# Optimization experiments

Measured on AMD Instinct MI355X. Metric: run time of the kernel, lower is better.

The kernel has to match this reference:

```python
import jax, jax.numpy as jnp
import numpy as np
import math

B, L, D, H, FACTOR = 4, 2048, 256, 8, 5
DH = D // H

def setup_inputs() -> dict:
    key = jax.random.key(0)
    ks = jax.random.split(key, 12)
    s = 1.0 / math.sqrt(D)
    return {
        "q": jax.random.normal(ks[0], (B, L, D), jnp.float32),
        "k": jax.random.normal(ks[1], (B, L, D), jnp.float32),
        "v": jax.random.normal(ks[2], (B, L, D), jnp.float32),
        "Wq": jax.random.normal(ks[3], (D, D), jnp.float32) * s,
        "bq": jax.random.normal(ks[4], (D,), jnp.float32) * s,
        "Wk": jax.random.normal(ks[5], (D, D), jnp.float32) * s,
        "bk": jax.random.normal(ks[6], (D,), jnp.float32) * s,
        "Wv": jax.random.normal(ks[7], (D, D), jnp.float32) * s,
        "bv": jax.random.normal(ks[8], (D,), jnp.float32) * s,
        "Wc": jax.random.normal(ks[9], (D, D), jnp.float32) * s,
        "bc": jax.random.normal(ks[10], (D,), jnp.float32) * s,
        "index_sample": jax.random.randint(ks[11], (L,), 0, L),  # U_part = min(5*L*ceil(log1p(L)), L) = L
    }

def reference(q, k, v, Wq, bq, Wk, bk, Wv, bv, Wc, bc, index_sample):
    # projections (torch Linear: x @ W^T + b)
    qp = q @ Wq.T + bq
    kp = k @ Wk.T + bk
    vp = v @ Wv.T + bv
    # NOTE: original reshapes q with a raw view (no transpose), k/v via split()
    q4 = qp.reshape(B, H, L, DH)                       # faithful to q.view(B, H, L, dh)
    k4 = kp.reshape(B, L, H, DH).transpose(0, 2, 1, 3)
    v4 = vp.reshape(B, L, H, DH).transpose(0, 2, 1, 3)
    qf = q4.reshape(B * H, L, DH)
    kf = k4.reshape(B * H, L, DH)
    vf = v4.reshape(B * H, L, DH)
    # random K sampling (with replacement); U_part == L here
    K_sample = kf[:, index_sample, :]                  # [BH, L, dh]
    QK = jnp.einsum('bld,bud->blu', qf, K_sample)      # [BH, L, L]
    M = QK.max(axis=-1) - QK.sum(axis=-1) / L          # sparsity measure [BH, L]
    u = min(FACTOR * math.ceil(math.log1p(L)), L)      # = 40
    _, top_idx = jax.lax.top_k(-M, u)                  # topk(..., largest=False)
    Q_red = jnp.take_along_axis(qf, top_idx[:, :, None], axis=1)  # [BH, u, dh]
    scores = jnp.einsum('bud,bld->bul', Q_red, kf) / math.sqrt(DH)
    probs = jax.nn.softmax(scores, axis=-1)
    out = jnp.einsum('bul,bld->bud', probs, vf)        # [BH, u, dh]
    out = out.reshape(B, H, u, DH).transpose(0, 2, 1, 3).reshape(B, u, D)
    return out @ Wc.T + bc
```

## Files before the change

kernel.cpp:

```cpp
#include <hip/hip_runtime.h>
#include <math.h>

#define B_ 4
#define L_ 2048
#define D_ 256
#define H_ 8
#define DH_ 32
#define NH_ 32
#define U_ 40
#define LD_ 524288

typedef __attribute__((ext_vector_type(8))) short short8;
typedef __attribute__((ext_vector_type(4))) float floatx4;

static __device__ __forceinline__ unsigned long long ullmin_(unsigned long long a, unsigned long long b) {
    return a < b ? a : b;
}
static __device__ __forceinline__ unsigned short f2bf_rne(float x) {
    unsigned u = __float_as_uint(x);
    unsigned r = u + 0x7FFFu + ((u >> 16) & 1u);
    return (unsigned short)(r >> 16);
}
static __device__ __forceinline__ float bf2f(unsigned short h) {
    return __uint_as_float(((unsigned)h) << 16);
}
// ... 106 lines not shown

#pragma unroll
    for (int mt = 0; mt < 2; ++mt)
#pragma unroll
        for (int nt = 0; nt < 4; ++nt) {
            const int c = colBase + nt * 16 + lq;
            const float bv_ = bias[c];
#pragma unroll
            for (int r = 0; r < 4; ++r) {
                const int mr = rowBaseW + mt * 16 + quad * 4 + r;
                Y[(size_t)mr * 256 + c] = acc[mt][nt][r] + bv_;
            }
        }
}

__global__ __launch_bounds__(256) void gemm_out(const float* __restrict__ X,
                                                const float* __restrict__ Wc,
                                                const float* __restrict__ bias,
                                                float* __restrict__ Y) {
    const int t = threadIdx.x;
    const int w = t >> 6, lane = t & 63;
    const int lq = lane & 15, quad = lane >> 4;
    const int colBase = blockIdx.y * 64;
    const int rowBaseW = blockIdx.x * 128 + w * 32;

    __shared__ unsigned short Bls[24576];

    floatx4 acc[2][4];
#pragma unroll
    for (int mt = 0; mt < 2; ++mt)
#pragma unroll
        for (int nt = 0; nt < 4; ++nt) acc[mt][nt] = (floatx4){0.f, 0.f, 0.f, 0.f};

    for (int phase = 0; phase < 2; ++phase) {
        __syncthreads();
#pragma unroll
        for (int r = 0; r < 8; ++r) {
            const int e = t + 256 * r;
            const int col = e >> 5;
            const int k4u = e & 31;
            const int kk = phase * 128 + k4u * 4;
            const float4 x = *(const float4*)(Wc + (size_t)(colBase + col) * 256 + kk);
            float xs[4] = {x.x, x.y, x.z, x.w};
            unsigned short hv[4], mv4[4], lv[4];
#pragma unroll
            for (int j = 0; j < 4; ++j) {
                hv[j] = f2bf_rne(xs[j]);
// ... 2 lines not shown
                const float e2 = e1 - bf2f(mv4[j]);
                lv[j] = f2bf_rne(e2);
            }
            const int nt = col >> 4, cin = col & 15;
            const int ktl = k4u >> 3, kin = (k4u & 7) * 4;
            const int base = nt * 512 + cin * 32 + kin;
            *(ushort4*)&Bls[((0 * 4 + ktl) << 11) + base] = make_ushort4(hv[0], hv[1], hv[2], hv[3]);
            *(ushort4*)&Bls[((1 * 4 + ktl) << 11) + base] = make_ushort4(mv4[0], mv4[1], mv4[2], mv4[3]);
            *(ushort4*)&Bls[((2 * 4 + ktl) << 11) + base] = make_ushort4(lv[0], lv[1], lv[2], lv[3]);
        }
        __syncthreads();

#pragma unroll
        for (int ktl = 0; ktl < 4; ++ktl) {
            const int kt = phase * 4 + ktl;
            short8 Bh[4], Bm[4], Bl[4];
            const int fo = lq * 32 + quad * 8;
#pragma unroll
            for (int j = 0; j < 4; ++j) {
                Bh[j] = *(const short8*)&Bls[((0 * 4 + ktl) << 11) + j * 512 + fo];
                Bm[j] = *(const short8*)&Bls[((1 * 4 + ktl) << 11) + j * 512 + fo];
                Bl[j] = *(const short8*)&Bls[((2 * 4 + ktl) << 11) + j * 512 + fo];
            }
#pragma unroll
            for (int mt = 0; mt < 2; ++mt) {
                const int m = rowBaseW + mt * 16 + lq;
                short8 Ah, Am, Al;
                {
                    float xs[8] = {0.f, 0.f, 0.f, 0.f, 0.f, 0.f, 0.f, 0.f};
                    if (m < 160) {
                        const float* xr = X + (size_t)m * 256 + kt * 32 + quad * 8;
                        const float4 x0 = *(const float4*)xr;
                        const float4 x1 = *(const float4*)(xr + 4);
                        xs[0] = x0.x; xs[1] = x0.y; xs[2] = x0.z; xs[3] = x0.w;
                        xs[4] = x1.x; xs[5] = x1.y; xs[6] = x1.z; xs[7] = x1.w;
                    }
#pragma unroll
                    for (int j = 0; j < 8; ++j) {
                        const unsigned short h = f2bf_rne(xs[j]);
                        const float e1 = xs[j] - bf2f(h);
                        const unsigned short md = f2bf_rne(e1);
                        const float e2 = e1 - bf2f(md);
                        Ah[j] = (short)h;
                        Am[j] = (short)md;
                        Al[j] = (short)f2bf_rne(e2);
                    }
                }
#pragma unroll
                for (int j = 0; j < 4; ++j) {
                    floatx4 a = acc[mt][j];
                    a = __builtin_amdgcn_mfma_f32_16x16x32_bf16(Am, Bm[j], a, 0, 0, 0);
                    a = __builtin_amdgcn_mfma_f32_16x16x32_bf16(Ah, Bl[j], a, 0, 0, 0);
                    a = __builtin_amdgcn_mfma_f32_16x16x32_bf16(Al, Bh[j], a, 0, 0, 0);
                    a = __builtin_amdgcn_mfma_f32_16x16x32_bf16(Ah, Bm[j], a, 0, 0, 0);
                    a = __builtin_amdgcn_mfma_f32_16x16x32_bf16(Am, Bh[j], a, 0, 0, 0);
                    a = __builtin_amdgcn_mfma_f32_16x16x32_bf16(Ah, Bh[j], a, 0, 0, 0);
                    acc[mt][j] = a;
                }
            }
        }
    }

#pragma unroll
    for (int mt = 0; mt < 2; ++mt)
#pragma unroll
        for (int nt = 0; nt < 4; ++nt) {
            const int c = colBase + nt * 16 + lq;
            const float bv = bias[c];
#pragma unroll
            for (int r = 0; r < 4; ++r) {
                const int mr = rowBaseW + mt * 16 + quad * 4 + r;
                if (mr < 160) Y[(size_t)mr * 256 + c] = acc[mt][nt][r] + bv;
            }
        }
}

__global__ __launch_bounds__(256) void kconv_ksum(const float* __restrict__ kp,
                                                  const int* __restrict__ idx,
                                                  unsigned short* __restrict__ Khi,
                                                  unsigned short* __restrict__ Klo,
                                                  float* __restrict__ Ksum8) {
    const int blk = blockIdx.x;
    const int i = blk >> 3, uc = blk & 7;
    const int b = i >> 3, h = i & 7;
    const int t = threadIdx.x;
    const int dq = (t & 7) * 4;
    const int ur = t >> 3;

    __shared__ float part[32][36];
    float ksum[4] = {0.f, 0.f, 0.f, 0.f};

#pragma unroll
    for (int p = 0; p < 8; ++p) {
        int u = uc * 256 + p * 32 + ur;
        const float4 x = *(const float4*)(kp + (size_t)b * LD_ + (size_t)idx[u] * D_ + h * DH_ + dq);
        float xs[4] = {x.x, x.y, x.z, x.w};
        unsigned short hv[4], lv[4];
#pragma unroll
        for (int j = 0; j < 4; ++j) {
            ksum[j] += xs[j];
            hv[j] = f2bf_rne(xs[j]);
            lv[j] = f2bf_rne(xs[j] - bf2f(hv[j]));
        }
        size_t o = ((size_t)i * 2048 + u) * 32 + dq;
        *(ushort4*)(Khi + o) = make_ushort4(hv[0], hv[1], hv[2], hv[3]);
        *(ushort4*)(Klo + o) = make_ushort4(lv[0], lv[1], lv[2], lv[3]);
    }
#pragma unroll
    for (int j = 0; j < 4; ++j) part[ur][dq + j] = ksum[j];
    __syncthreads();
    if (t < 32) {
        float s = 0.f;
#pragma unroll 8
        for (int u2 = 0; u2 < 32; ++u2) s += part[u2][t];
        Ksum8[(size_t)blk * 32 + t] = s;
    }
}

__global__ __launch_bounds__(256) void mpart_mfma(const float* __restrict__ qp,
                                                  const unsigned short* __restrict__ Khi,
                                                  const unsigned short* __restrict__ Klo,
                                                  const float* __restrict__ Ksum8,
                                                  float* __restrict__ Mv,
                                                  float* __restrict__ Qmean) {
    const int blk = blockIdx.x;
    const int i = blk >> 5;
    const int lg = blk & 31;
    const int t = threadIdx.x;
    const int w = t >> 6;
    const int lane = t & 63;
    const int lq = lane & 15;
    const int quad = lane >> 4;

    __shared__ float ssum[32];
    __shared__ float red[4][64];
    if (t < 32) {
        float s = 0.f;
#pragma unroll
        for (int uc = 0; uc < 8; ++uc) s += Ksum8[((size_t)i * 8 + uc) * 32 + t];
        ssum[t] = s;
    }

    short8 Ah[4], Al[4];
#pragma unroll
    for (int lt = 0; lt < 4; ++lt) {
        const int l = lg * 64 + lt * 16 + lq;
        const float* qrow = qp + ((size_t)i * 2048 + l) * 32 + quad * 8;
        float4 x0 = *(const float4*)(qrow);
        float4 x1 = *(const float4*)(qrow + 4);
        float xs[8] = {x0.x, x0.y, x0.z, x0.w, x1.x, x1.y, x1.z, x1.w};
#pragma unroll
        for (int j = 0; j < 8; ++j) {
            unsigned short h = f2bf_rne(xs[j]);
            unsigned short lo = f2bf_rne(xs[j] - bf2f(h));
            Ah[lt][j] = (short)h;
            Al[lt][j] = (short)lo;
        }
    }

    floatx4 rmax[4];
#pragma unroll
    for (int lt = 0; lt < 4; ++lt)
        rmax[lt] = (floatx4){-INFINITY, -INFINITY, -INFINITY, -INFINITY};

    const size_t kfrag = ((size_t)i * 2048 + w * 512 + lq) * 32 + quad * 8;
    const unsigned short* ph = Khi + kfrag;
    const unsigned short* pl = Klo + kfrag;
#pragma unroll 2
    for (int s = 0; s < 32; ++s) {
        short8 Bh = *(const short8*)(ph + (size_t)s * 512);
        short8 Bl = *(const short8*)(pl + (size_t)s * 512);
#pragma unroll
        for (int lt = 0; lt < 4; ++lt) {
            floatx4 acc = (floatx4){0.f, 0.f, 0.f, 0.f};
            acc = __builtin_amdgcn_mfma_f32_16x16x32_bf16(Al[lt], Bh, acc, 0, 0, 0);
            acc = __builtin_amdgcn_mfma_f32_16x16x32_bf16(Ah[lt], Bl, acc, 0, 0, 0);
            acc = __builtin_amdgcn_mfma_f32_16x16x32_bf16(Ah[lt], Bh, acc, 0, 0, 0);
#pragma unroll
            for (int r = 0; r < 4; ++r) rmax[lt][r] = fmaxf(rmax[lt][r], acc[r]);
        }
    }

#pragma unroll
    for (int lt = 0; lt < 4; ++lt)
#pragma unroll
        for (int r = 0; r < 4; ++r) {
            float v = rmax[lt][r];
#pragma unroll
            for (int off = 1; off < 16; off <<= 1)
                v = fmaxf(v, __shfl_xor(v, off, 64));
            rmax[lt][r] = v;
        }
    if (lq == 0) {
#pragma unroll
        for (int lt = 0; lt < 4; ++lt)
#pragma unroll
            for (int r = 0; r < 4; ++r)
                red[w][lt * 16 + quad * 4 + r] = rmax[lt][r];
    }
    __syncthreads();
    if (t < 64) {
        const int l = lg * 64 + t;
        float m = fmaxf(fmaxf(red[0][t], red[1][t]), fmaxf(red[2][t], red[3][t]));
        const float4* q4 = (const float4*)(qp + ((size_t)i * 2048 + l) * 32);
        const float4* s4 = (const float4*)ssum;
        float qs = 0.f;
#pragma unroll
        for (int z = 0; z < 8; ++z) {
            float4 a = q4[z];
            float4 c = s4[z];
            qs = fmaf(a.x, c.x, qs);
            qs = fmaf(a.y, c.y, qs);
            qs = fmaf(a.z, c.z, qs);
            qs = fmaf(a.w, c.w, qs);
        }
        const float qm = qs * (1.0f / 2048.0f);
        Qmean[(size_t)i * 2048 + l] = qm;
        Mv[(size_t)i * 2048 + l] = m - qm;
    }
}

__global__ __launch_bounds__(256) void topk64_kernel(const float* __restrict__ Mv,
                                                     int* __restrict__ candIdx) {
    const int i = blockIdx.x;
    const int t = threadIdx.x;
    unsigned long long keys[8];
    __shared__ unsigned long long wred[4];
#pragma unroll
    for (int j = 0; j < 8; ++j) {
        const int l = t + 256 * j;
        unsigned u32 = __float_as_uint(Mv[(size_t)i * 2048 + l]);
        u32 = (u32 & 0x80000000u) ? ~u32 : (u32 | 0x80000000u);
        keys[j] = ((unsigned long long)u32 << 32) | (unsigned)l;
    }
    for (int it = 0; it < 64; ++it) {
        unsigned long long best = keys[0];
#pragma unroll
        for (int j = 1; j < 8; ++j) best = ullmin_(best, keys[j]);
#pragma unroll
        for (int off = 1; off < 64; off <<= 1)
            best = ullmin_(best, __shfl_xor(best, off, 64));
        if ((t & 63) == 0) wred[t >> 6] = best;
        __syncthreads();
        const unsigned long long m = ullmin_(ullmin_(wred[0], wred[1]), ullmin_(wred[2], wred[3]));
        if (t == 0) candIdx[i * 64 + it] = (int)(m & 0xffffffffu);
#pragma unroll
        for (int j = 0; j < 8; ++j)
            if (keys[j] == m) keys[j] = ~0ULL;
        __syncthreads();
    }
}

__global__ __launch_bounds__(256) void refine_kernel(const float* __restrict__ qp,
                                                     const float* __restrict__ kp,
                                                     const int* __restrict__ idx,
                                                     const int* __restrict__ candIdx,
                                                     float* __restrict__ refPart) {
    const int blk = blockIdx.x;
    const int i = blk >> 3, c = blk & 7;
    const int b = i >> 3, h = i & 7;
    const int t = threadIdx.x;
    __shared__ float qc[64][40];
    __shared__ float Ks[128][40];

    {
        const int cand = t >> 2, dp = (t & 3) * 8;
        const int l = candIdx[i * 64 + cand];
        const float* src = qp + ((size_t)i * 2048 + l) * 32 + dp;
        *(float4*)&qc[cand][dp] = *(const float4*)(src);
        *(float4*)&qc[cand][dp + 4] = *(const float4*)(src + 4);
    }
    __syncthreads();

    const int cand = t >> 2, usub = t & 3;
    float qv[32];
#pragma unroll
    for (int z = 0; z < 8; ++z) {
        float4 a = *(const float4*)&qc[cand][z * 4];
        qv[4 * z] = a.x; qv[4 * z + 1] = a.y; qv[4 * z + 2] = a.z; qv[4 * z + 3] = a.w;
    }

    float m = -INFINITY;
    for (int s = 0; s < 2; ++s) {
        {
            const int r = t >> 1, half = t & 1;
            const int u = c * 256 + s * 128 + r;
            const float* krow = kp + (size_t)b * LD_ + (size_t)idx[u] * D_ + h * DH_ + half * 16;
#pragma unroll
            for (int z = 0; z < 4; ++z)
                *(float4*)&Ks[r][half * 16 + z * 4] = *(const float4*)(krow + z * 4);
        }
        __syncthreads();
        for (int ur = usub; ur < 128; ur += 4) {
            float a0 = 0, a1 = 0, a2 = 0, a3 = 0;
#pragma unroll
            for (int z = 0; z < 8; ++z) {
                float4 kv = *(const float4*)&Ks[ur][z * 4];
                a0 = fmaf(qv[4 * z], kv.x, a0);
                a1 = fmaf(qv[4 * z + 1], kv.y, a1);
                a2 = fmaf(qv[4 * z + 2], kv.z, a2);
                a3 = fmaf(qv[4 * z + 3], kv.w, a3);
            }
            m = fmaxf(m, (a0 + a1) + (a2 + a3));
        }
        __syncthreads();
    }
    m = fmaxf(m, __shfl_xor(m, 1, 64));
    m = fmaxf(m, __shfl_xor(m, 2, 64));
    if ((t & 3) == 0) refPart[((size_t)i * 8 + c) * 64 + cand] = m;
}

__global__ __launch_bounds__(64) void select40_kernel(const int* __restrict__ candIdx,
                                                      const float* __restrict__ refPart,
                                                      const float* __restrict__ Qmean,
                                                      int* __restrict__ topIdx) {
    const int i = blockIdx.x;
    const int t = threadIdx.x;
    const int l = candIdx[i * 64 + t];
    float m = -INFINITY;
#pragma unroll
    for (int c = 0; c < 8; ++c) m = fmaxf(m, refPart[((size_t)i * 8 + c) * 64 + t]);
    float Mex = m - Qmean[(size_t)i * 2048 + l];
    unsigned u32 = __float_as_uint(Mex);
    u32 = (u32 & 0x80000000u) ? ~u32 : (u32 | 0x80000000u);
    unsigned long long key = ((unsigned long long)u32 << 32) | (unsigned)l;
    for (int it = 0; it < 40; ++it) {
        unsigned long long k2 = key;
#pragma unroll
        for (int off = 1; off < 64; off <<= 1) k2 = ullmin_(k2, __shfl_xor(k2, off, 64));
        if (key == k2) {
            topIdx[i * 40 + it] = l;
            key = ~0ULL;
        }
    }
}

#define SCP 258
#define VSP 36

__global__ __launch_bounds__(320) void attn_part(const float* __restrict__ qp,
                                                 const float* __restrict__ kp,
                                                 const float* __restrict__ vp,
                                                 const int* __restrict__ topIdx,
                                                 float* __restrict__ mPart,
                                                 float* __restrict__ sPart,
                                                 float* __restrict__ oPart) {
    const int blk = blockIdx.x;
    const int i = blk >> 3, c = blk & 7;
    const int b = i >> 3, h = i & 7;
    const int t = threadIdx.x;

    __shared__ float Qs[40][32];
    __shared__ float Vs[256][VSP];
    __shared__ float sc[40][SCP];
    __shared__ float mred[40], sred[40];

    {
        const int r = t >> 3, qq = t & 7;
        const int lq = topIdx[i * 40 + r];
        *(float4*)&Qs[r][qq * 4] = *(const float4*)(qp + ((size_t)i * 2048 + lq) * 32 + qq * 4);
    }
    for (int e = t; e < 2048; e += 320) {
        const int r = e >> 3, qq = e & 7;
        *(float4*)&Vs[r][qq * 4] =
            *(const float4*)(vp + (size_t)b * LD_ + (size_t)(c * 256 + r) * 256 + h * 32 + qq * 4);
    }
    __syncthreads();

    const float scale = 0.17677669529663687f;

    if (t < 256) {
        const float* kr = kp + (size_t)b * LD_ + (size_t)(c * 256 + t) * 256 + h * 32;
        float kv[32];
#pragma unroll
        for (int z = 0; z < 8; ++z) {
            float4 x = *(const float4*)(kr + z * 4);
            kv[4 * z] = x.x; kv[4 * z + 1] = x.y; kv[4 * z + 2] = x.z; kv[4 * z + 3] = x.w;
        }
#pragma unroll 4
        for (int j = 0; j < 40; ++j) {
            float a0 = 0, a1 = 0, a2 = 0, a3 = 0;
#pragma unroll
            for (int z = 0; z < 8; ++z) {
                const float4 q4 = *(const float4*)&Qs[j][z * 4];
                a0 = fmaf(kv[4 * z], q4.x, a0);
                a1 = fmaf(kv[4 * z + 1], q4.y, a1);
                a2 = fmaf(kv[4 * z + 2], q4.z, a2);
                a3 = fmaf(kv[4 * z + 3], q4.w, a3);
            }
            sc[j][t] = ((a0 + a1) + (a2 + a3)) * scale;
        }
    }
    __syncthreads();

    {
        const int w = t >> 6, lane = t & 63;
#pragma unroll
        for (int r = 0; r < 8; ++r) {
            const int j = w * 8 + r;
            float x0 = sc[j][lane], x1 = sc[j][lane + 64];
            float x2 = sc[j][lane + 128], x3 = sc[j][lane + 192];
            float m = fmaxf(fmaxf(x0, x1), fmaxf(x2, x3));
#pragma unroll
            for (int off = 1; off < 64; off <<= 1) m = fmaxf(m, __shfl_xor(m, off, 64));
            const float e0 = __expf(x0 - m), e1 = __expf(x1 - m);
            const float e2 = __expf(x2 - m), e3 = __expf(x3 - m);
            sc[j][lane] = e0; sc[j][lane + 64] = e1;
            sc[j][lane + 128] = e2; sc[j][lane + 192] = e3;
            float s = (e0 + e1) + (e2 + e3);
#pragma unroll
            for (int off = 1; off < 64; off <<= 1) s += __shfl_xor(s, off, 64);
            if (lane == 0) { mred[j] = m; sred[j] = s; }
        }
    }
    __syncthreads();

    {
        const int j = t >> 3, qq = t & 7;
        float4 acc = make_float4(0.f, 0.f, 0.f, 0.f);
        for (int l = 0; l < 256; ++l) {
            const float p = sc[j][l];
            const float4 v4 = *(const float4*)&Vs[l][qq * 4];
            acc.x = fmaf(p, v4.x, acc.x);
            acc.y = fmaf(p, v4.y, acc.y);
            acc.z = fmaf(p, v4.z, acc.z);
            acc.w = fmaf(p, v4.w, acc.w);
        }
        const size_t o = (size_t)(i * 8 + c) * 40 + j;
        *(float4*)&oPart[o * 32 + qq * 4] = acc;
        if (qq == 0) { mPart[o] = mred[j]; sPart[o] = sred[j]; }
    }
}

__global__ __launch_bounds__(256) void attn_combine(const float* __restrict__ mPart,
                                                    const float* __restrict__ sPart,
                                                    const float* __restrict__ oPart,
                                                    float* __restrict__ attnOut) {
    const int i = blockIdx.x;
    const int b = i >> 3, h = i & 7;
    const int t = threadIdx.x;
    for (int e = t; e < 1280; e += 256) {
        const int j = e >> 5, d = e & 31;
        float mv[8];
        float M = -INFINITY;
#pragma unroll
        for (int c = 0; c < 8; ++c) {
            mv[c] = mPart[(size_t)(i * 8 + c) * 40 + j];
            M = fmaxf(M, mv[c]);
        }
        float S = 0.f, O = 0.f;
#pragma unroll
        for (int c = 0; c < 8; ++c) {
            const float sc_ = __expf(mv[c] - M);
            const size_t o = (size_t)(i * 8 + c) * 40 + j;
            S = fmaf(sPart[o], sc_, S);
            O = fmaf(oPart[o * 32 + d], sc_, O);
        }
        attnOut[((size_t)b * 40 + j) * 256 + h * 32 + d] = O / S;
    }
}

extern "C" void kernel_launch(void* const* d_in, const int* in_sizes, int n_in,
                              void* d_out, int out_size, void* d_ws, size_t ws_size,
                              hipStream_t stream) {
    const float* q  = (const float*)d_in[0];
    const float* k  = (const float*)d_in[1];
    const float* v  = (const float*)d_in[2];
    const float* Wq = (const float*)d_in[3];
    const float* bq = (const float*)d_in[4];
    const float* Wk = (const float*)d_in[5];
    const float* bk = (const float*)d_in[6];
    const float* Wv = (const float*)d_in[7];
    const float* bv = (const float*)d_in[8];
    const float* Wc = (const float*)d_in[9];
    const float* bc = (const float*)d_in[10];
    const int* idx  = (const int*)d_in[11];
    float* out = (float*)d_out;

    char* w = (char*)d_ws;
    float*          qp      = (float*)(w);
    float*          kp      = (float*)(w + (8u << 20));
    float*          vp      = (float*)(w + (16u << 20));
    unsigned short* Khi     = (unsigned short*)(w + (24u << 20));
    unsigned short* Klo     = (unsigned short*)(w + (28u << 20));
    float*          Mv      = (float*)(w + (32u << 20));
    float*          Qmean   = (float*)(w + (32u << 20) + (256u << 10));
    float*          Ksum8   = (float*)(w + (32u << 20) + (512u << 10));
    int*            candIdx = (int*)  (w + (32u << 20) + (544u << 10));
    int*            topIdx  = (int*)  (w + (32u << 20) + (552u << 10));
    float*          attnOut = (float*)(w + (32u << 20) + (560u << 10));
    float*          refPart = (float*)(w + (32u << 20) + (720u << 10));
    float*          mPart   = (float*)(w + (24u << 20));
    float*          sPart   = (float*)(w + (24u << 20) + (64u << 10));
    float*          oPart   = (float*)(w + (24u << 20) + (128u << 10));

    hipLaunchKernelGGL(gemm_mfma3, dim3(64, 4, 3), dim3(256), 0, stream,
                       q, k, v, Wq, Wk, Wv, bq, bk, bv, qp, kp, vp);
    hipLaunchKernelGGL(kconv_ksum, dim3(256), dim3(256), 0, stream, kp, idx, Khi, Klo, Ksum8);
    hipLaunchKernelGGL(mpart_mfma, dim3(1024), dim3(256), 0, stream, qp, Khi, Klo, Ksum8, Mv, Qmean);
    hipLaunchKernelGGL(topk64_kernel, dim3(32), dim3(256), 0, stream, Mv, candIdx);
    hipLaunchKernelGGL(refine_kernel, dim3(256), dim3(256), 0, stream, qp, kp, idx, candIdx, refPart);
    hipLaunchKernelGGL(select40_kernel, dim3(32), dim3(64), 0, stream, candIdx, refPart, Qmean, topIdx);
    hipLaunchKernelGGL(attn_part, dim3(256), dim3(320), 0, stream, qp, kp, vp, topIdx, mPart, sPart, oPart);
    hipLaunchKernelGGL(attn_combine, dim3(32), dim3(256), 0, stream, mPart, sPart, oPart, attnOut);
    hipLaunchKernelGGL(gemm_out, dim3(2, 4), dim3(256), 0, stream, attnOut, Wc, bc, out);
}
```

Measured before the change: 256.1 us.

## Fuse attention combine into output GEMM and split K/attention work finer

Folds the attn_combine kernel into gemm_out, so each block merges the partial softmax results for one batch into shared memory before running the output projection. This removes one launch and the attnOut round trip. kconv_ksum now uses 1024 blocks with 32 partial key sums, and attn_part now uses 16 chunks of 128 keys, to raise parallelism on a small grid. The cost is redundant combine work across the column blocks of gemm_out and more partial data to reduce.

```diff
diff --git a/kernel.cpp b/kernel.cpp
--- a/kernel.cpp
+++ b/kernel.cpp
@@ -9,6 +9,7 @@
 #define NH_ 32
 #define U_ 40
 #define LD_ 524288
+#define NCH_ 16
 
 typedef __attribute__((ext_vector_type(8))) short short8;
 typedef __attribute__((ext_vector_type(4))) float floatx4;
@@ -145,23 +146,411 @@
         }
 }
 
-__global__ __launch_bounds__(256) void gemm_out(const float* __restrict__ X,
+__global__ __launch_bounds__(256) void kconv_ksum(const float* __restrict__ kp,
+                                                  const int* __restrict__ idx,
+                                                  unsigned short* __restrict__ Khi,
+                                                  unsigned short* __restrict__ Klo,
+                                                  float* __restrict__ Ksum32) {
+    const int blk = blockIdx.x;
+    const int i = blk >> 5, uc = blk & 31;
+    const int b = i >> 3, h = i & 7;
+    const int t = threadIdx.x;
+    const int dq = (t & 7) * 4;
+    const int ur = t >> 3;
+
+    __shared__ float part[32][36];
+    float ksum[4] = {0.f, 0.f, 0.f, 0.f};
+
+#pragma unroll
+    for (int p = 0; p < 2; ++p) {
+        int u = uc * 64 + p * 32 + ur;
+        const float4 x = *(const float4*)(kp + (size_t)b * LD_ + (size_t)idx[u] * D_ + h * DH_ + dq);
+        float xs[4] = {x.x, x.y, x.z, x.w};
+        unsigned short hv[4], lv[4];
+#pragma unroll
+        for (int j = 0; j < 4; ++j) {
+            ksum[j] += xs[j];
+            hv[j] = f2bf_rne(xs[j]);
+            lv[j] = f2bf_rne(xs[j] - bf2f(hv[j]));
+        }
+        size_t o = ((size_t)i * 2048 + u) * 32 + dq;
+        *(ushort4*)(Khi + o) = make_ushort4(hv[0], hv[1], hv[2], hv[3]);
+        *(ushort4*)(Klo + o) = make_ushort4(lv[0], lv[1], lv[2], lv[3]);
+    }
+#pragma unroll
+    for (int j = 0; j < 4; ++j) part[ur][dq + j] = ksum[j];
+    __syncthreads();
+    if (t < 32) {
+        float s = 0.f;
+#pragma unroll 8
+        for (int u2 = 0; u2 < 32; ++u2) s += part[u2][t];
+        Ksum32[(size_t)blk * 32 + t] = s;
+    }
+}
+
+__global__ __launch_bounds__(256) void mpart_mfma(const float* __restrict__ qp,
+                                                  const unsigned short* __restrict__ Khi,
+                                                  const unsigned short* __restrict__ Klo,
+                                                  const float* __restrict__ Ksum32,
+                                                  float* __restrict__ Mv,
+                                                  float* __restrict__ Qmean) {
+    const int blk = blockIdx.x;
+    const int i = blk >> 5;
+    const int lg = blk & 31;
+    const int t = threadIdx.x;
+    const int w = t >> 6;
+    const int lane = t & 63;
+    const int lq = lane & 15;
+    const int quad = lane >> 4;
+
+    __shared__ float ssum[32];
+    __shared__ float red[4][64];
+    if (t < 32) {
+        float s = 0.f;
+#pragma unroll 8
+        for (int uc = 0; uc < 32; ++uc) s += Ksum32[((size_t)i * 32 + uc) * 32 + t];
+        ssum[t] = s;
+    }
+
+    short8 Ah[4], Al[4];
+#pragma unroll
+    for (int lt = 0; lt < 4; ++lt) {
+        const int l = lg * 64 + lt * 16 + lq;
+        const float* qrow = qp + ((size_t)i * 2048 + l) * 32 + quad * 8;
+        float4 x0 = *(const float4*)(qrow);
+        float4 x1 = *(const float4*)(qrow + 4);
+        float xs[8] = {x0.x, x0.y, x0.z, x0.w, x1.x, x1.y, x1.z, x1.w};
+#pragma unroll
+        for (int j = 0; j < 8; ++j) {
+            unsigned short h = f2bf_rne(xs[j]);
+            unsigned short lo = f2bf_rne(xs[j] - bf2f(h));
+            Ah[lt][j] = (short)h;
+            Al[lt][j] = (short)lo;
+        }
+    }
+
+    floatx4 rmax[4];
+#pragma unroll
+    for (int lt = 0; lt < 4; ++lt)
+        rmax[lt] = (floatx4){-INFINITY, -INFINITY, -INFINITY, -INFINITY};
+
+    const size_t kfrag = ((size_t)i * 2048 + w * 512 + lq) * 32 + quad * 8;
+    const unsigned short* ph = Khi + kfrag;
+    const unsigned short* pl = Klo + kfrag;
+#pragma unroll 2
+    for (int s = 0; s < 32; ++s) {
+        short8 Bh = *(const short8*)(ph + (size_t)s * 512);
+        short8 Bl = *(const short8*)(pl + (size_t)s * 512);
+#pragma unroll
+        for (int lt = 0; lt < 4; ++lt) {
+            floatx4 acc = (floatx4){0.f, 0.f, 0.f, 0.f};
+            acc = __builtin_amdgcn_mfma_f32_16x16x32_bf16(Al[lt], Bh, acc, 0, 0, 0);
+            acc = __builtin_amdgcn_mfma_f32_16x16x32_bf16(Ah[lt], Bl, acc, 0, 0, 0);
+            acc = __builtin_amdgcn_mfma_f32_16x16x32_bf16(Ah[lt], Bh, acc, 0, 0, 0);
+#pragma unroll
+            for (int r = 0; r < 4; ++r) rmax[lt][r] = fmaxf(rmax[lt][r], acc[r]);
+        }
+    }
+
+#pragma unroll
+    for (int lt = 0; lt < 4; ++lt)
+#pragma unroll
+        for (int r = 0; r < 4; ++r) {
+            float v = rmax[lt][r];
+#pragma unroll
+            for (int off = 1; off < 16; off <<= 1)
+                v = fmaxf(v, __shfl_xor(v, off, 64));
+            rmax[lt][r] = v;
+        }
+    if (lq == 0) {
+#pragma unroll
+        for (int lt = 0; lt < 4; ++lt)
+#pragma unroll
+            for (int r = 0; r < 4; ++r)
+                red[w][lt * 16 + quad * 4 + r] = rmax[lt][r];
+    }
+    __syncthreads();
+    if (t < 64) {
+        const int l = lg * 64 + t;
+        float m = fmaxf(fmaxf(red[0][t], red[1][t]), fmaxf(red[2][t], red[3][t]));
+        const float4* q4 = (const float4*)(qp + ((size_t)i * 2048 + l) * 32);
+        const float4* s4 = (const float4*)ssum;
+        float qs = 0.f;
+#pragma unroll
+        for (int z = 0; z < 8; ++z) {
+            float4 a = q4[z];
+            float4 c = s4[z];
+            qs = fmaf(a.x, c.x, qs);
+            qs = fmaf(a.y, c.y, qs);
+            qs = fmaf(a.z, c.z, qs);
+            qs = fmaf(a.w, c.w, qs);
+        }
+        const float qm = qs * (1.0f / 2048.0f);
+        Qmean[(size_t)i * 2048 + l] = qm;
+        Mv[(size_t)i * 2048 + l] = m - qm;
+    }
+}
+
+__global__ __launch_bounds__(256) void topk64_kernel(const float* __restrict__ Mv,
+                                                     int* __restrict__ candIdx) {
+    const int i = blockIdx.x;
+    const int t = threadIdx.x;
+    unsigned long long keys[8];
+    __shared__ unsigned long long wred[4];
+#pragma unroll
+    for (int j = 0; j < 8; ++j) {
+        const int l = t + 256 * j;
+        unsigned u32 = __float_as_uint(Mv[(size_t)i * 2048 + l]);
+        u32 = (u32 & 0x80000000u) ? ~u32 : (u32 | 0x80000000u);
+        keys[j] = ((unsigned long long)u32 << 32) | (unsigned)l;
+    }
+    for (int it = 0; it < 64; ++it) {
+        unsigned long long best = keys[0];
+#pragma unroll
+        for (int j = 1; j < 8; ++j) best = ullmin_(best, keys[j]);
+#pragma unroll
+        for (int off = 1; off < 64; off <<= 1)
+            best = ullmin_(best, __shfl_xor(best, off, 64));
+        if ((t & 63) == 0) wred[t >> 6] = best;
+        __syncthreads();
+        const unsigned long long m = ullmin_(ullmin_(wred[0], wred[1]), ullmin_(wred[2], wred[3]));
+        if (t == 0) candIdx[i * 64 + it] = (int)(m & 0xffffffffu);
+#pragma unroll
+        for (int j = 0; j < 8; ++j)
+            if (keys[j] == m) keys[j] = ~0ULL;
+        __syncthreads();
+    }
+}
+
+__global__ __launch_bounds__(256) void refine_kernel(const float* __restrict__ qp,
+                                                     const float* __restrict__ kp,
+                                                     const int* __restrict__ idx,
+                                                     const int* __restrict__ candIdx,
+                                                     float* __restrict__ refPart) {
+    const int blk = blockIdx.x;
+    const int i = blk >> 3, c = blk & 7;
+    const int b = i >> 3, h = i & 7;
+    const int t = threadIdx.x;
+    __shared__ float qc[64][40];
+    __shared__ float Ks[128][40];
+
+    {
+        const int cand = t >> 2, dp = (t & 3) * 8;
+        const int l = candIdx[i * 64 + cand];
+        const float* src = qp + ((size_t)i * 2048 + l) * 32 + dp;
+        *(float4*)&qc[cand][dp] = *(const float4*)(src);
+        *(float4*)&qc[cand][dp + 4] = *(const float4*)(src + 4);
+    }
+    __syncthreads();
+
+    const int cand = t >> 2, usub = t & 3;
+    float qv[32];
+#pragma unroll
+    for (int z = 0; z < 8; ++z) {
+        float4 a = *(const float4*)&qc[cand][z * 4];
+        qv[4 * z] = a.x; qv[4 * z + 1] = a.y; qv[4 * z + 2] = a.z; qv[4 * z + 3] = a.w;
+    }
+
+    float m = -INFINITY;
+    for (int s = 0; s < 2; ++s) {
+        {
+            const int r = t >> 1, half = t & 1;
+            const int u = c * 256 + s * 128 + r;
+            const float* krow = kp + (size_t)b * LD_ + (size_t)idx[u] * D_ + h * DH_ + half * 16;
+#pragma unroll
+            for (int z = 0; z < 4; ++z)
+                *(float4*)&Ks[r][half * 16 + z * 4] = *(const float4*)(krow + z * 4);
+        }
+        __syncthreads();
+        for (int ur = usub; ur < 128; ur += 4) {
+            float a0 = 0, a1 = 0, a2 = 0, a3 = 0;
+#pragma unroll
+            for (int z = 0; z < 8; ++z) {
+                float4 kv = *(const float4*)&Ks[ur][z * 4];
+                a0 = fmaf(qv[4 * z], kv.x, a0);
+                a1 = fmaf(qv[4 * z + 1], kv.y, a1);
+                a2 = fmaf(qv[4 * z + 2], kv.z, a2);
+                a3 = fmaf(qv[4 * z + 3], kv.w, a3);
+            }
+            m = fmaxf(m, (a0 + a1) + (a2 + a3));
+        }
+        __syncthreads();
+    }
+    m = fmaxf(m, __shfl_xor(m, 1, 64));
+    m = fmaxf(m, __shfl_xor(m, 2, 64));
+    if ((t & 3) == 0) refPart[((size_t)i * 8 + c) * 64 + cand] = m;
+}
+
+__global__ __launch_bounds__(64) void select40_kernel(const int* __restrict__ candIdx,
+                                                      const float* __restrict__ refPart,
+                                                      const float* __restrict__ Qmean,
+                                                      int* __restrict__ topIdx) {
+    const int i = blockIdx.x;
+    const int t = threadIdx.x;
+    const int l = candIdx[i * 64 + t];
+    float m = -INFINITY;
+#pragma unroll
+    for (int c = 0; c < 8; ++c) m = fmaxf(m, refPart[((size_t)i * 8 + c) * 64 + t]);
+    float Mex = m - Qmean[(size_t)i * 2048 + l];
+    unsigned u32 = __float_as_uint(Mex);
+    u32 = (u32 & 0x80000000u) ? ~u32 : (u32 | 0x80000000u);
+    unsigned long long key = ((unsigned long long)u32 << 32) | (unsigned)l;
+    for (int it = 0; it < 40; ++it) {
+        unsigned long long k2 = key;
+#pragma unroll
+        for (int off = 1; off < 64; off <<= 1) k2 = ullmin_(k2, __shfl_xor(k2, off, 64));
+        if (key == k2) {
+            topIdx[i * 40 + it] = l;
+            key = ~0ULL;
+        }
+    }
+}
+
+#define SCP2 136
+#define VSP 36
+
+__global__ __launch_bounds__(320) void attn_part(const float* __restrict__ qp,
+                                                 const float* __restrict__ kp,
+                                                 const float* __restrict__ vp,
+                                                 const int* __restrict__ topIdx,
+                                                 float* __restrict__ mPart,
+                                                 float* __restrict__ sPart,
+                                                 float* __restrict__ oPart) {
+    const int blk = blockIdx.x;
+    const int i = blk >> 4, c = blk & 15;
+    const int b = i >> 3, h = i & 7;
+    const int t = threadIdx.x;
+
+    __shared__ float Qs[40][32];
+    __shared__ float Vs[128][VSP];
+    __shared__ float sc[40][SCP2];
+    __shared__ float mred[40], sred[40];
+
+    {
+        const int r = t >> 3, qq = t & 7;
+        const int lq = topIdx[i * 40 + r];
+        *(float4*)&Qs[r][qq * 4] = *(const float4*)(qp + ((size_t)i * 2048 + lq) * 32 + qq * 4);
+    }
+    for (int e = t; e < 1024; e += 320) {
+        const int r = e >> 3, qq = e & 7;
+        *(float4*)&Vs[r][qq * 4] =
+            *(const float4*)(vp + (size_t)b * LD_ + (size_t)(c * 128 + r) * 256 + h * 32 + qq * 4);
+    }
+    __syncthreads();
+
+    const float scale = 0.17677669529663687f;
+
+    if (t < 256) {
+        const int r = t >> 1;
+        const int j0 = (t & 1) * 20;
+        const float* kr = kp + (size_t)b * LD_ + (size_t)(c * 128 + r) * 256 + h * 32;
+        float kv[32];
+#pragma unroll
+        for (int z = 0; z < 8; ++z) {
+            float4 x = *(const float4*)(kr + z * 4);
+            kv[4 * z] = x.x; kv[4 * z + 1] = x.y; kv[4 * z + 2] = x.z; kv[4 * z + 3] = x.w;
+        }
+#pragma unroll 4
+        for (int jj = 0; jj < 20; ++jj) {
+            const int j = j0 + jj;
+            float a0 = 0, a1 = 0, a2 = 0, a3 = 0;
+#pragma unroll
+            for (int z = 0; z < 8; ++z) {
+                const float4 q4 = *(const float4*)&Qs[j][z * 4];
+                a0 = fmaf(kv[4 * z], q4.x, a0);
+                a1 = fmaf(kv[4 * z + 1], q4.y, a1);
+                a2 = fmaf(kv[4 * z + 2], q4.z, a2);
+                a3 = fmaf(kv[4 * z + 3], q4.w, a3);
+            }
+            sc[j][r] = ((a0 + a1) + (a2 + a3)) * scale;
+        }
+    }
+    __syncthreads();
+
+    {
+        const int w = t >> 6, lane = t & 63;
+#pragma unroll
+        for (int rr = 0; rr < 8; ++rr) {
+            const int j = w * 8 + rr;
+            float x0 = sc[j][lane], x1 = sc[j][lane + 64];
+            float m = fmaxf(x0, x1);
+#pragma unroll
+            for (int off = 1; off < 64; off <<= 1) m = fmaxf(m, __shfl_xor(m, off, 64));
+            const float e0 = __expf(x0 - m), e1 = __expf(x1 - m);
+            sc[j][lane] = e0; sc[j][lane + 64] = e1;
+            float s = e0 + e1;
+#pragma unroll
+            for (int off = 1; off < 64; off <<= 1) s += __shfl_xor(s, off, 64);
+            if (lane == 0) { mred[j] = m; sred[j] = s; }
+        }
+    }
+    __syncthreads();
+
+    {
+        const int j = t >> 3, qq = t & 7;
+        float4 acc = make_float4(0.f, 0.f, 0.f, 0.f);
+        for (int l = 0; l < 128; ++l) {
+            const float p = sc[j][l];
+            const float4 v4 = *(const float4*)&Vs[l][qq * 4];
+            acc.x = fmaf(p, v4.x, acc.x);
+            acc.y = fmaf(p, v4.y, acc.y);
+            acc.z = fmaf(p, v4.z, acc.z);
+            acc.w = fmaf(p, v4.w, acc.w);
+        }
+        const size_t o = (size_t)(i * NCH_ + c) * 40 + j;
+        *(float4*)&oPart[o * 32 + qq * 4] = acc;
+        if (qq == 0) { mPart[o] = mred[j]; sPart[o] = sred[j]; }
+    }
+}
+
+__global__ __launch_bounds__(256) void gemm_out(const float* __restrict__ mPart,
+                                                const float* __restrict__ sPart,
+                                                const float* __restrict__ oPart,
                                                 const float* __restrict__ Wc,
                                                 const float* __restrict__ bias,
-                                                float* __restrict__ Y) {
+                                                float* __restrict__ out) {
+    const int b = blockIdx.x;
+    const int colBase = blockIdx.y * 64;
     const int t = threadIdx.x;
     const int w = t >> 6, lane = t & 63;
     const int lq = lane & 15, quad = lane >> 4;
-    const int colBase = blockIdx.y * 64;
-    const int rowBaseW = blockIdx.x * 128 + w * 32;
-
+
+    __shared__ float Xs[40][258];
     __shared__ unsigned short Bls[24576];
 
-    floatx4 acc[2][4];
-#pragma unroll
-    for (int mt = 0; mt < 2; ++mt)
-#pragma unroll
-        for (int nt = 0; nt < 4; ++nt) acc[mt][nt] = (floatx4){0.f, 0.f, 0.f, 0.f};
+    for (int e = t; e < 320; e += 256) {
+        const int j = e >> 3, h = e & 7;
+        const int i = b * 8 + h;
+        const size_t base = (size_t)i * NCH_ * 40 + j;
+        float mv[NCH_];
+        float M = -INFINITY;
+#pragma unroll
+        for (int c = 0; c < NCH_; ++c) {
+            mv[c] = mPart[base + (size_t)c * 40];
+            M = fmaxf(M, mv[c]);
+        }
+        float wgt[NCH_];
+        float S = 0.f;
+#pragma unroll
+        for (int c = 0; c < NCH_; ++c) {
+            wgt[c] = __expf(mv[c] - M);
+            S = fmaf(sPart[base + (size_t)c * 40], wgt[c], S);
+        }
+        const float invS = 1.0f / S;
+#pragma unroll 4
+        for (int d = 0; d < 32; ++d) {
+            float O = 0.f;
+#pragma unroll
+            for (int c = 0; c < NCH_; ++c)
+                O = fmaf(oPart[(base + (size_t)c * 40) * 32 + d], wgt[c], O);
+            Xs[j][h * 32 + d] = O * invS;
+        }
+    }
+    __syncthreads();
+
+    floatx4 acc[3];
+#pragma unroll
+    for (int mt = 0; mt < 3; ++mt) acc[mt] = (floatx4){0.f, 0.f, 0.f, 0.f};
 
     for (int phase = 0; phase < 2; ++phase) {
         __syncthreads();
@@ -194,22 +583,19 @@
 #pragma unroll
         for (int ktl = 0; ktl < 4; ++ktl) {
             const int kt = phase * 4 + ktl;
-            short8 Bh[4], Bm[4], Bl[4];
-            const int fo = lq * 32 + quad * 8;
-#pragma unroll
-            for (int j = 0; j < 4; ++j) {
-                Bh[j] = *(const short8*)&Bls[((0 * 4 + ktl) << 11) + j * 512 + fo];
-                Bm[j] = *(const short8*)&Bls[((1 * 4 + ktl) << 11) + j * 512 + fo];
-                Bl[j] = *(const short8*)&Bls[((2 * 4 + ktl) << 11) + j * 512 + fo];
-            }
-#pragma unroll
-            for (int mt = 0; mt < 2; ++mt) {
-                const int m = rowBaseW + mt * 16 + lq;
+            short8 Bh, Bm, Bl;
+            const int fo = w * 512 + lq * 32 + quad * 8;
+            Bh = *(const short8*)&Bls[((0 * 4 + ktl) << 11) + fo];
+            Bm = *(const short8*)&Bls[((1 * 4 + ktl) << 11) + fo];
+            Bl = *(const short8*)&Bls[((2 * 4 + ktl) << 11) + fo];
+#pragma unroll
+            for (int mt = 0; mt < 3; ++mt) {
+                const int m = mt * 16 + lq;
                 short8 Ah, Am, Al;
                 {
                     float xs[8] = {0.f, 0.f, 0.f, 0.f, 0.f, 0.f, 0.f, 0.f};
-                    if (m < 160) {
-                        const float* xr = X + (size_t)m * 256 + kt * 32 + quad * 8;
+                    if (m < 40) {
+                        const float* xr = &Xs[m][kt * 32 + quad * 8];
                         const float4 x0 = *(const float4*)xr;
                         const float4 x1 = *(const float4*)(xr + 4);
                         xs[0] = x0.x; xs[1] = x0.y; xs[2] = x0.z; xs[3] = x0.w;
@@ -226,417 +612,27 @@
                         Al[j] = (short)f2bf_rne(e2);
                     }
                 }
-#pragma unroll
-                for (int j = 0; j < 4; ++j) {
-                    floatx4 a = acc[mt][j];
-                    a = __builtin_amdgcn_mfma_f32_16x16x32_bf16(Am, Bm[j], a, 0, 0, 0);
-                    a = __builtin_amdgcn_mfma_f32_16x16x32_bf16(Ah, Bl[j], a, 0, 0, 0);
-                    a = __builtin_amdgcn_mfma_f32_16x16x32_bf16(Al, Bh[j], a, 0, 0, 0);
-                    a = __builtin_amdgcn_mfma_f32_16x16x32_bf16(Ah, Bm[j], a, 0, 0, 0);
-                    a = __builtin_amdgcn_mfma_f32_16x16x32_bf16(Am, Bh[j], a, 0, 0, 0);
-                    a = __builtin_amdgcn_mfma_f32_16x16x32_bf16(Ah, Bh[j], a, 0, 0, 0);
-                    acc[mt][j] = a;
-                }
-            }
-        }
-    }
-
-#pragma unroll
-    for (int mt = 0; mt < 2; ++mt)
-#pragma unroll
-        for (int nt = 0; nt < 4; ++nt) {
-            const int c = colBase + nt * 16 + lq;
-            const float bv = bias[c];
-#pragma unroll
-            for (int r = 0; r < 4; ++r) {
-                const int mr = rowBaseW + mt * 16 + quad * 4 + r;
-                if (mr < 160) Y[(size_t)mr * 256 + c] = acc[mt][nt][r] + bv;
-            }
-        }
-}
-
-__global__ __launch_bounds__(256) void kconv_ksum(const float* __restrict__ kp,
-                                                  const int* __restrict__ idx,
-                                                  unsigned short* __restrict__ Khi,
-                                                  unsigned short* __restrict__ Klo,
-                                                  float* __restrict__ Ksum8) {
-    const int blk = blockIdx.x;
-    const int i = blk >> 3, uc = blk & 7;
-    const int b = i >> 3, h = i & 7;
-    const int t = threadIdx.x;
-    const int dq = (t & 7) * 4;
-    const int ur = t >> 3;
-
-    __shared__ float part[32][36];
-    float ksum[4] = {0.f, 0.f, 0.f, 0.f};
-
-#pragma unroll
-    for (int p = 0; p < 8; ++p) {
-        int u = uc * 256 + p * 32 + ur;
-        const float4 x = *(const float4*)(kp + (size_t)b * LD_ + (size_t)idx[u] * D_ + h * DH_ + dq);
-        float xs[4] = {x.x, x.y, x.z, x.w};
-        unsigned short hv[4], lv[4];
-#pragma unroll
-        for (int j = 0; j < 4; ++j) {
-            ksum[j] += xs[j];
-            hv[j] = f2bf_rne(xs[j]);
-            lv[j] = f2bf_rne(xs[j] - bf2f(hv[j]));
-        }
-        size_t o = ((size_t)i * 2048 + u) * 32 + dq;
-        *(ushort4*)(Khi + o) = make_ushort4(hv[0], hv[1], hv[2], hv[3]);
-        *(ushort4*)(Klo + o) = make_ushort4(lv[0], lv[1], lv[2], lv[3]);
-    }
-#pragma unroll
-    for (int j = 0; j < 4; ++j) part[ur][dq + j] = ksum[j];
-    __syncthreads();
-    if (t < 32) {
-        float s = 0.f;
-#pragma unroll 8
-        for (int u2 = 0; u2 < 32; ++u2) s += part[u2][t];
-        Ksum8[(size_t)blk * 32 + t] = s;
-    }
-}
-
-__global__ __launch_bounds__(256) void mpart_mfma(const float* __restrict__ qp,
-                                                  const unsigned short* __restrict__ Khi,
-                                                  const unsigned short* __restrict__ Klo,
-                                                  const float* __restrict__ Ksum8,
-                                                  float* __restrict__ Mv,
-                                                  float* __restrict__ Qmean) {
-    const int blk = blockIdx.x;
-    const int i = blk >> 5;
-    const int lg = blk & 31;
-    const int t = threadIdx.x;
-    const int w = t >> 6;
-    const int lane = t & 63;
-    const int lq = lane & 15;
-    const int quad = lane >> 4;
-
-    __shared__ float ssum[32];
-    __shared__ float red[4][64];
-    if (t < 32) {
-        float s = 0.f;
-#pragma unroll
-        for (int uc = 0; uc < 8; ++uc) s += Ksum8[((size_t)i * 8 + uc) * 32 + t];
-        ssum[t] = s;
-    }
-
-    short8 Ah[4], Al[4];
-#pragma unroll
-    for (int lt = 0; lt < 4; ++lt) {
-        const int l = lg * 64 + lt * 16 + lq;
-        const float* qrow = qp + ((size_t)i * 2048 + l) * 32 + quad * 8;
-        float4 x0 = *(const float4*)(qrow);
-        float4 x1 = *(const float4*)(qrow + 4);
-        float xs[8] = {x0.x, x0.y, x0.z, x0.w, x1.x, x1.y, x1.z, x1.w};
-#pragma unroll
-        for (int j = 0; j < 8; ++j) {
-            unsigned short h = f2bf_rne(xs[j]);
-            unsigned short lo = f2bf_rne(xs[j] - bf2f(h));
-            Ah[lt][j] = (short)h;
-            Al[lt][j] = (short)lo;
-        }
-    }
-
-    floatx4 rmax[4];
-#pragma unroll
-    for (int lt = 0; lt < 4; ++lt)
-        rmax[lt] = (floatx4){-INFINITY, -INFINITY, -INFINITY, -INFINITY};
-
-    const size_t kfrag = ((size_t)i * 2048 + w * 512 + lq) * 32 + quad * 8;
-    const unsigned short* ph = Khi + kfrag;
-    const unsigned short* pl = Klo + kfrag;
-#pragma unroll 2
-    for (int s = 0; s < 32; ++s) {
-        short8 Bh = *(const short8*)(ph + (size_t)s * 512);
-        short8 Bl = *(const short8*)(pl + (size_t)s * 512);
-#pragma unroll
-        for (int lt = 0; lt < 4; ++lt) {
-            floatx4 acc = (floatx4){0.f, 0.f, 0.f, 0.f};
-            acc = __builtin_amdgcn_mfma_f32_16x16x32_bf16(Al[lt], Bh, acc, 0, 0, 0);
-            acc = __builtin_amdgcn_mfma_f32_16x16x32_bf16(Ah[lt], Bl, acc, 0, 0, 0);
-            acc = __builtin_amdgcn_mfma_f32_16x16x32_bf16(Ah[lt], Bh, acc, 0, 0, 0);
-#pragma unroll
-            for (int r = 0; r < 4; ++r) rmax[lt][r] = fmaxf(rmax[lt][r], acc[r]);
-        }
-    }
-
-#pragma unroll
-    for (int lt = 0; lt < 4; ++lt)
+                floatx4 a = acc[mt];
+                a = __builtin_amdgcn_mfma_f32_16x16x32_bf16(Am, Bm, a, 0, 0, 0);
+                a = __builtin_amdgcn_mfma_f32_16x16x32_bf16(Ah, Bl, a, 0, 0, 0);
+                a = __builtin_amdgcn_mfma_f32_16x16x32_bf16(Al, Bh, a, 0, 0, 0);
+                a = __builtin_amdgcn_mfma_f32_16x16x32_bf16(Ah, Bm, a, 0, 0, 0);
+                a = __builtin_amdgcn_mfma_f32_16x16x32_bf16(Am, Bh, a, 0, 0, 0);
+                a = __builtin_amdgcn_mfma_f32_16x16x32_bf16(Ah, Bh, a, 0, 0, 0);
+                acc[mt] = a;
+            }
+        }
+    }
+
+#pragma unroll
+    for (int mt = 0; mt < 3; ++mt) {
+        const int cc = colBase + w * 16 + lq;
+        const float bv = bias[cc];
 #pragma unroll
         for (int r = 0; r < 4; ++r) {
-            float v = rmax[lt][r];
-#pragma unroll
-            for (int off = 1; off < 16; off <<= 1)
-                v = fmaxf(v, __shfl_xor(v, off, 64));
-            rmax[lt][r] = v;
-        }
-    if (lq == 0) {
-#pragma unroll
-        for (int lt = 0; lt < 4; ++lt)
-#pragma unroll
-            for (int r = 0; r < 4; ++r)
-                red[w][lt * 16 + quad * 4 + r] = rmax[lt][r];
-    }
-    __syncthreads();
-    if (t < 64) {
-        const int l = lg * 64 + t;
-        float m = fmaxf(fmaxf(red[0][t], red[1][t]), fmaxf(red[2][t], red[3][t]));
-        const float4* q4 = (const float4*)(qp + ((size_t)i * 2048 + l) * 32);
-        const float4* s4 = (const float4*)ssum;
-        float qs = 0.f;
-#pragma unroll
-        for (int z = 0; z < 8; ++z) {
-            float4 a = q4[z];
-            float4 c = s4[z];
-            qs = fmaf(a.x, c.x, qs);
-            qs = fmaf(a.y, c.y, qs);
-            qs = fmaf(a.z, c.z, qs);
-            qs = fmaf(a.w, c.w, qs);
-        }
-        const float qm = qs * (1.0f / 2048.0f);
-        Qmean[(size_t)i * 2048 + l] = qm;
-        Mv[(size_t)i * 2048 + l] = m - qm;
-    }
-}
-
-__global__ __launch_bounds__(256) void topk64_kernel(const float* __restrict__ Mv,
-                                                     int* __restrict__ candIdx) {
-    const int i = blockIdx.x;
-    const int t = threadIdx.x;
-    unsigned long long keys[8];
-    __shared__ unsigned long long wred[4];
-#pragma unroll
-    for (int j = 0; j < 8; ++j) {
-        const int l = t + 256 * j;
-        unsigned u32 = __float_as_uint(Mv[(size_t)i * 2048 + l]);
-        u32 = (u32 & 0x80000000u) ? ~u32 : (u32 | 0x80000000u);
-        keys[j] = ((unsigned long long)u32 << 32) | (unsigned)l;
-    }
-    for (int it = 0; it < 64; ++it) {
-        unsigned long long best = keys[0];
-#pragma unroll
-        for (int j = 1; j < 8; ++j) best = ullmin_(best, keys[j]);
-#pragma unroll
-        for (int off = 1; off < 64; off <<= 1)
-            best = ullmin_(best, __shfl_xor(best, off, 64));
-        if ((t & 63) == 0) wred[t >> 6] = best;
-        __syncthreads();
-        const unsigned long long m = ullmin_(ullmin_(wred[0], wred[1]), ullmin_(wred[2], wred[3]));
-        if (t == 0) candIdx[i * 64 + it] = (int)(m & 0xffffffffu);
-#pragma unroll
-        for (int j = 0; j < 8; ++j)
-            if (keys[j] == m) keys[j] = ~0ULL;
-        __syncthreads();
-    }
-}
-
-__global__ __launch_bounds__(256) void refine_kernel(const float* __restrict__ qp,
-                                                     const float* __restrict__ kp,
-                                                     const int* __restrict__ idx,
-                                                     const int* __restrict__ candIdx,
-                                                     float* __restrict__ refPart) {
-    const int blk = blockIdx.x;
-    const int i = blk >> 3, c = blk & 7;
-    const int b = i >> 3, h = i & 7;
-    const int t = threadIdx.x;
-    __shared__ float qc[64][40];
-    __shared__ float Ks[128][40];
-
-    {
-        const int cand = t >> 2, dp = (t & 3) * 8;
-        const int l = candIdx[i * 64 + cand];
-        const float* src = qp + ((size_t)i * 2048 + l) * 32 + dp;
-        *(float4*)&qc[cand][dp] = *(const float4*)(src);
-        *(float4*)&qc[cand][dp + 4] = *(const float4*)(src + 4);
-    }
-    __syncthreads();
-
-    const int cand = t >> 2, usub = t & 3;
-    float qv[32];
-#pragma unroll
-    for (int z = 0; z < 8; ++z) {
-        float4 a = *(const float4*)&qc[cand][z * 4];
-        qv[4 * z] = a.x; qv[4 * z + 1] = a.y; qv[4 * z + 2] = a.z; qv[4 * z + 3] = a.w;
-    }
-
-    float m = -INFINITY;
-    for (int s = 0; s < 2; ++s) {
-        {
-            const int r = t >> 1, half = t & 1;
-            const int u = c * 256 + s * 128 + r;
-            const float* krow = kp + (size_t)b * LD_ + (size_t)idx[u] * D_ + h * DH_ + half * 16;
-#pragma unroll
-            for (int z = 0; z < 4; ++z)
-                *(float4*)&Ks[r][half * 16 + z * 4] = *(const float4*)(krow + z * 4);
-        }
-        __syncthreads();
-        for (int ur = usub; ur < 128; ur += 4) {
-            float a0 = 0, a1 = 0, a2 = 0, a3 = 0;
-#pragma unroll
-            for (int z = 0; z < 8; ++z) {
-                float4 kv = *(const float4*)&Ks[ur][z * 4];
-                a0 = fmaf(qv[4 * z], kv.x, a0);
-                a1 = fmaf(qv[4 * z + 1], kv.y, a1);
-                a2 = fmaf(qv[4 * z + 2], kv.z, a2);
-                a3 = fmaf(qv[4 * z + 3], kv.w, a3);
-            }
-            m = fmaxf(m, (a0 + a1) + (a2 + a3));
-        }
-        __syncthreads();
-    }
-    m = fmaxf(m, __shfl_xor(m, 1, 64));
-    m = fmaxf(m, __shfl_xor(m, 2, 64));
-    if ((t & 3) == 0) refPart[((size_t)i * 8 + c) * 64 + cand] = m;
-}
-
-__global__ __launch_bounds__(64) void select40_kernel(const int* __restrict__ candIdx,
-                                                      const float* __restrict__ refPart,
-                                                      const float* __restrict__ Qmean,
-                                                      int* __restrict__ topIdx) {
-    const int i = blockIdx.x;
-    const int t = threadIdx.x;
-    const int l = candIdx[i * 64 + t];
-    float m = -INFINITY;
-#pragma unroll
-    for (int c = 0; c < 8; ++c) m = fmaxf(m, refPart[((size_t)i * 8 + c) * 64 + t]);
-    float Mex = m - Qmean[(size_t)i * 2048 + l];
-    unsigned u32 = __float_as_uint(Mex);
-    u32 = (u32 & 0x80000000u) ? ~u32 : (u32 | 0x80000000u);
-    unsigned long long key = ((unsigned long long)u32 << 32) | (unsigned)l;
-    for (int it = 0; it < 40; ++it) {
-        unsigned long long k2 = key;
-#pragma unroll
-        for (int off = 1; off < 64; off <<= 1) k2 = ullmin_(k2, __shfl_xor(k2, off, 64));
-        if (key == k2) {
-            topIdx[i * 40 + it] = l;
-            key = ~0ULL;
-        }
-    }
-}
-
-#define SCP 258
-#define VSP 36
-
-__global__ __launch_bounds__(320) void attn_part(const float* __restrict__ qp,
-                                                 const float* __restrict__ kp,
-                                                 const float* __restrict__ vp,
-                                                 const int* __restrict__ topIdx,
-                                                 float* __restrict__ mPart,
-                                                 float* __restrict__ sPart,
-                                                 float* __restrict__ oPart) {
-    const int blk = blockIdx.x;
-    const int i = blk >> 3, c = blk & 7;
-    const int b = i >> 3, h = i & 7;
-    const int t = threadIdx.x;
-
-    __shared__ float Qs[40][32];
-    __shared__ float Vs[256][VSP];
-    __shared__ float sc[40][SCP];
-    __shared__ float mred[40], sred[40];
-
-    {
-        const int r = t >> 3, qq = t & 7;
-        const int lq = topIdx[i * 40 + r];
-        *(float4*)&Qs[r][qq * 4] = *(const float4*)(qp + ((size_t)i * 2048 + lq) * 32 + qq * 4);
-    }
-    for (int e = t; e < 2048; e += 320) {
-        const int r = e >> 3, qq = e & 7;
-        *(float4*)&Vs[r][qq * 4] =
-            *(const float4*)(vp + (size_t)b * LD_ + (size_t)(c * 256 + r) * 256 + h * 32 + qq * 4);
-    }
-    __syncthreads();
-
-    const float scale = 0.17677669529663687f;
-
-    if (t < 256) {
-        const float* kr = kp + (size_t)b * LD_ + (size_t)(c * 256 + t) * 256 + h * 32;
-        float kv[32];
-#pragma unroll
-        for (int z = 0; z < 8; ++z) {
-            float4 x = *(const float4*)(kr + z * 4);
-            kv[4 * z] = x.x; kv[4 * z + 1] = x.y; kv[4 * z + 2] = x.z; kv[4 * z + 3] = x.w;
-        }
-#pragma unroll 4
-        for (int j = 0; j < 40; ++j) {
-            float a0 = 0, a1 = 0, a2 = 0, a3 = 0;
-#pragma unroll
-            for (int z = 0; z < 8; ++z) {
-                const float4 q4 = *(const float4*)&Qs[j][z * 4];
-                a0 = fmaf(kv[4 * z], q4.x, a0);
-                a1 = fmaf(kv[4 * z + 1], q4.y, a1);
-                a2 = fmaf(kv[4 * z + 2], q4.z, a2);
-                a3 = fmaf(kv[4 * z + 3], q4.w, a3);
-            }
-            sc[j][t] = ((a0 + a1) + (a2 + a3)) * scale;
-        }
-    }
-    __syncthreads();
-
-    {
-        const int w = t >> 6, lane = t & 63;
-#pragma unroll
-        for (int r = 0; r < 8; ++r) {
-            const int j = w * 8 + r;
-            float x0 = sc[j][lane], x1 = sc[j][lane + 64];
-            float x2 = sc[j][lane + 128], x3 = sc[j][lane + 192];
-            float m = fmaxf(fmaxf(x0, x1), fmaxf(x2, x3));
-#pragma unroll
-            for (int off = 1; off < 64; off <<= 1) m = fmaxf(m, __shfl_xor(m, off, 64));
-            const float e0 = __expf(x0 - m), e1 = __expf(x1 - m);
-            const float e2 = __expf(x2 - m), e3 = __expf(x3 - m);
-            sc[j][lane] = e0; sc[j][lane + 64] = e1;
-            sc[j][lane + 128] = e2; sc[j][lane + 192] = e3;
-            float s = (e0 + e1) + (e2 + e3);
-#pragma unroll
-            for (int off = 1; off < 64; off <<= 1) s += __shfl_xor(s, off, 64);
-            if (lane == 0) { mred[j] = m; sred[j] = s; }
-        }
-    }
-    __syncthreads();
-
-    {
-        const int j = t >> 3, qq = t & 7;
-        float4 acc = make_float4(0.f, 0.f, 0.f, 0.f);
-        for (int l = 0; l < 256; ++l) {
-            const float p = sc[j][l];
-            const float4 v4 = *(const float4*)&Vs[l][qq * 4];
-            acc.x = fmaf(p, v4.x, acc.x);
-            acc.y = fmaf(p, v4.y, acc.y);
-            acc.z = fmaf(p, v4.z, acc.z);
-            acc.w = fmaf(p, v4.w, acc.w);
-        }
-        const size_t o = (size_t)(i * 8 + c) * 40 + j;
-        *(float4*)&oPart[o * 32 + qq * 4] = acc;
-        if (qq == 0) { mPart[o] = mred[j]; sPart[o] = sred[j]; }
-    }
-}
-
-__global__ __launch_bounds__(256) void attn_combine(const float* __restrict__ mPart,
-                                                    const float* __restrict__ sPart,
-                                                    const float* __restrict__ oPart,
-                                                    float* __restrict__ attnOut) {
-    const int i = blockIdx.x;
-    const int b = i >> 3, h = i & 7;
-    const int t = threadIdx.x;
-    for (int e = t; e < 1280; e += 256) {
-        const int j = e >> 5, d = e & 31;
-        float mv[8];
-        float M = -INFINITY;
-#pragma unroll
-        for (int c = 0; c < 8; ++c) {
-            mv[c] = mPart[(size_t)(i * 8 + c) * 40 + j];
-            M = fmaxf(M, mv[c]);
-        }
-        float S = 0.f, O = 0.f;
-#pragma unroll
-        for (int c = 0; c < 8; ++c) {
-            const float sc_ = __expf(mv[c] - M);
-            const size_t o = (size_t)(i * 8 + c) * 40 + j;
-            S = fmaf(sPart[o], sc_, S);
-            O = fmaf(oPart[o * 32 + d], sc_, O);
-        }
-        attnOut[((size_t)b * 40 + j) * 256 + h * 32 + d] = O / S;
+            const int ml = mt * 16 + quad * 4 + r;
+            if (ml < 40) out[(size_t)(b * 40 + ml) * 256 + cc] = acc[mt][r] + bv;
+        }
     }
 }
 
@@ -665,23 +661,21 @@
     unsigned short* Klo     = (unsigned short*)(w + (28u << 20));
     float*          Mv      = (float*)(w + (32u << 20));
     float*          Qmean   = (float*)(w + (32u << 20) + (256u << 10));
-    float*          Ksum8   = (float*)(w + (32u << 20) + (512u << 10));
-    int*            candIdx = (int*)  (w + (32u << 20) + (544u << 10));
-    int*            topIdx  = (int*)  (w + (32u << 20) + (552u << 10));
-    float*          attnOut = (float*)(w + (32u << 20) + (560u << 10));
-    float*          refPart = (float*)(w + (32u << 20) + (720u << 10));
+    float*          Ksum32  = (float*)(w + (32u << 20) + (512u << 10));
+    int*            candIdx = (int*)  (w + (32u << 20) + (640u << 10));
+    int*            topIdx  = (int*)  (w + (32u << 20) + (648u << 10));
+    float*          refPart = (float*)(w + (32u << 20) + (656u << 10));
     float*          mPart   = (float*)(w + (24u << 20));
-    float*          sPart   = (float*)(w + (24u << 20) + (64u << 10));
-    float*          oPart   = (float*)(w + (24u << 20) + (128u << 10));
+    float*          sPart   = (float*)(w + (24u << 20) + (128u << 10));
+    float*          oPart   = (float*)(w + (24u << 20) + (256u << 10));
 
     hipLaunchKernelGGL(gemm_mfma3, dim3(64, 4, 3), dim3(256), 0, stream,
                        q, k, v, Wq, Wk, Wv, bq, bk, bv, qp, kp, vp);
-    hipLaunchKernelGGL(kconv_ksum, dim3(256), dim3(256), 0, stream, kp, idx, Khi, Klo, Ksum8);
-    hipLaunchKernelGGL(mpart_mfma, dim3(1024), dim3(256), 0, stream, qp, Khi, Klo, Ksum8, Mv, Qmean);
+    hipLaunchKernelGGL(kconv_ksum, dim3(1024), dim3(256), 0, stream, kp, idx, Khi, Klo, Ksum32);
+    hipLaunchKernelGGL(mpart_mfma, dim3(1024), dim3(256), 0, stream, qp, Khi, Klo, Ksum32, Mv, Qmean);
     hipLaunchKernelGGL(topk64_kernel, dim3(32), dim3(256), 0, stream, Mv, candIdx);
     hipLaunchKernelGGL(refine_kernel, dim3(256), dim3(256), 0, stream, qp, kp, idx, candIdx, refPart);
     hipLaunchKernelGGL(select40_kernel, dim3(32), dim3(64), 0, stream, candIdx, refPart, Qmean, topIdx);
-    hipLaunchKernelGGL(attn_part, dim3(256), dim3(320), 0, stream, qp, kp, vp, topIdx, mPart, sPart, oPart);
-    hipLaunchKernelGGL(attn_combine, dim3(32), dim3(256), 0, stream, mPart, sPart, oPart, attnOut);
-    hipLaunchKernelGGL(gemm_out, dim3(2, 4), dim3(256), 0, stream, attnOut, Wc, bc, out);
-}
+    hipLaunchKernelGGL(attn_part, dim3(512), dim3(320), 0, stream, qp, kp, vp, topIdx, mPart, sPart, oPart);
+    hipLaunchKernelGGL(gemm_out, dim3(4, 4), dim3(256), 0, stream, mPart, sPart, oPart, Wc, bc, out);
+}
```

New measurement: 266.1 us. 1.04x slower.
